# Kernel optimization log

Measured on AMD Instinct MI355X. Metric: run time of the kernel, lower is better.

The kernel has to match this reference:

```python
import jax, jax.numpy as jnp
import numpy as np

IN_CH, EMBED_DIM, N_CODES = 8, 64, 512


def conv1d(x, w, b, stride, pad):
    # x: [B,C,T], w: [O,I,K] (torch Conv1d layout)
    y = jax.lax.conv_general_dilated(x, w, (stride,), [(pad, pad)],
                                     dimension_numbers=('NCH', 'OIH', 'NCH'))
    return y + b[None, :, None]


def conv_transpose1d(x, w, b, stride, pad):
    # w: [I,O,K] (torch ConvTranspose1d layout); equiv to lhs-dilated conv with flipped kernel
    k = w.shape[2]
    wf = jnp.flip(jnp.transpose(w, (1, 0, 2)), axis=2)  # [O,I,K]
    y = jax.lax.conv_general_dilated(x, wf, (1,), [(k - 1 - pad, k - 1 - pad)],
                                     lhs_dilation=(stride,),
                                     dimension_numbers=('NCH', 'OIH', 'NCH'))
    return y + b[None, :, None]


def setup_inputs() -> dict:
    key = jax.random.key(0)
    ks = jax.random.split(key, 16)
    def p(k, shape, fan_in):
        lim = 1.0 / np.sqrt(fan_in)
        return jax.random.uniform(k, shape, jnp.float32, -lim, lim)
    x = jax.random.normal(ks[0], (16, IN_CH, 32768), jnp.float32)
    # encoder convs (torch Conv1d: [out,in,k])
    w1 = p(ks[1], (64, IN_CH, 7), IN_CH * 7);   b1 = p(ks[2], (64,), IN_CH * 7)
    w2 = p(ks[3], (128, 64, 5), 64 * 5);        b2 = p(ks[4], (128,), 64 * 5)
    w3 = p(ks[5], (EMBED_DIM, 128, 3), 128 * 3); b3 = p(ks[6], (EMBED_DIM,), 128 * 3)
    codebook = jax.random.uniform(ks[7], (N_CODES, EMBED_DIM), jnp.float32,
                                  -1.0 / N_CODES, 1.0 / N_CODES)
    # decoder conv-transposes (torch ConvTranspose1d: [in,out,k])
    dw1 = p(ks[8], (EMBED_DIM, 128, 4), EMBED_DIM * 4); db1 = p(ks[9], (128,), EMBED_DIM * 4)
    dw2 = p(ks[10], (128, 64, 4), 128 * 4);             db2 = p(ks[11], (64,), 128 * 4)
    dw3 = p(ks[12], (64, IN_CH, 4), 64 * 4);            db3 = p(ks[13], (IN_CH,), 64 * 4)
    return {'x': x, 'w1': w1, 'b1': b1, 'w2': w2, 'b2': b2, 'w3': w3, 'b3': b3,
            'codebook': codebook, 'dw1': dw1, 'db1': db1, 'dw2': dw2, 'db2': db2,
            'dw3': dw3, 'db3': db3}


def quantize(z_e, codebook):
    # z_e: [B,D,T]
    B, D, T = z_e.shape
    z_flat = jnp.transpose(z_e, (0, 2, 1)).reshape(-1, D)  # [B*T, D]
    # squared euclidean distances [B*T, n_codes]
    d2 = (jnp.sum(z_flat * z_flat, axis=1, keepdims=True)
          - 2.0 * z_flat @ codebook.T
          + jnp.sum(codebook * codebook, axis=1)[None, :])
    indices = jnp.argmin(d2, axis=1)
    z_q = codebook[indices].reshape(B, T, D).transpose(0, 2, 1)  # [B,D,T]
    return z_q, indices.reshape(B, T)


def mse(a, b):
    d = a - b
    return jnp.mean(d * d)


def reference(x, w1, b1, w2, b2, w3, b3, codebook, dw1, db1, dw2, db2, dw3, db3):
    sg = jax.lax.stop_gradient
    z = jax.nn.relu(conv1d(x, w1, b1, 2, 3))
    z = jax.nn.relu(conv1d(z, w2, b2, 2, 2))
    z_e = conv1d(z, w3, b3, 2, 1)  # [B, D, T/8]
    z_q, indices = quantize(z_e, codebook)
    z_q_st = z_e + sg(z_q - z_e)  # straight-through
    r = jax.nn.relu(conv_transpose1d(z_q_st, dw1, db1, 2, 1))
    r = jax.nn.relu(conv_transpose1d(r, dw2, db2, 2, 1))
    x_recon = conv_transpose1d(r, dw3, db3, 2, 1)  # [B, C, T]
    vq_loss = mse(sg(z_q), z_e)
    commitment_loss = mse(sg(z_e), z_q)
    T = min(x.shape[-1], x_recon.shape[-1])
    recon_loss = mse(x_recon[..., :T], x[..., :T])
    conditioning = jnp.mean(z_q_st, axis=-1)  # [B, D]
    return conditioning, vq_loss, commitment_loss, recon_loss
```

## Files before the change

kernel.cpp:

```cpp
#include <hip/hip_runtime.h>
#include <hip/hip_bf16.h>


#define NB 16
#define T0 32768
#define T1 16384
#define T2 8192
#define T3 4096
#define NCODES 512
#define EDIM 64

typedef __attribute__((ext_vector_type(8)))  short short8;
typedef __attribute__((ext_vector_type(16))) float f32x16;
typedef __attribute__((ext_vector_type(16))) unsigned u32x16;
typedef __attribute__((ext_vector_type(4)))  float f32x4;

__device__ __forceinline__ float b2f(short s) {
    unsigned u = ((unsigned)(unsigned short)s) << 16;
    float f; __builtin_memcpy(&f, &u, 4); return f;
}
__device__ __forceinline__ short f2bs(float f) {
    __hip_bfloat16 h = __float2bfloat16(f);
    short s; __builtin_memcpy(&s, &h, 2); return s;
}
__device__ __forceinline__ unsigned f2ord(float s) {
    unsigned u = __float_as_uint(s);
    return u ^ ((unsigned)((int)u >> 31) | 0x80000000u);
}

__device__ __forceinline__ void gload_lds16(const void* g, void* l) {
    __builtin_amdgcn_global_load_lds(
        (const __attribute__((address_space(1))) void*)g,
        (__attribute__((address_space(3))) void*)l, 16, 0, 0);
}

__device__ __forceinline__ float block_sum256(float v) {
    #pragma unroll
    for (int off = 32; off > 0; off >>= 1) v += __shfl_down(v, off, 64);
    __shared__ float red[4];
    int lane = threadIdx.x & 63, wv = threadIdx.x >> 6;
    if (lane == 0) red[wv] = v;
    __syncthreads();
    return red[0] + red[1] + red[2] + red[3];
}

__global__ __launch_bounds__(256, 2)
void conv1_mfma(const float* __restrict__ x, const short* __restrict__ w1b,
                const float* __restrict__ b1, short* __restrict__ y) {
    constexpr int BT = 128, NR = 262;
    __shared__ short lxc[NR * 8];
    __shared__ short lw[64 * 64];
    int tid = threadIdx.x, b = blockIdx.z, t0 = blockIdx.x * BT;
    for (int i = tid; i < 512; i += 256) {
        int oc = i >> 3, c8 = i & 7;
        short8 v = *(const short8*)(w1b + oc * 64 + c8 * 8);
        *(short8*)(lw + oc * 64 + (c8 ^ (oc & 7)) * 8) = v;
    }
    for (int r = tid; r < NR; r += 256) {
        int g = 2 * t0 - 3 + r;
        short8 p;
        bool ok = (unsigned)g < (unsigned)T0;
        #pragma unroll
        for (int ic = 0; ic < 8; ic++) {
            float v = ok ? x[((size_t)b * 8 + ic) * T0 + g] : 0.f;
            p[ic] = f2bs(v);
        }
        *(short8*)(lxc + r * 8) = p;
    }
    __syncthreads();
    int wv = tid >> 6, lane = tid & 63, lm = lane & 31, lk = lane >> 5;
    int ml = wv * 32 + lm;
    f32x16 acc[2];
    #pragma unroll
    for (int oj = 0; oj < 2; oj++)
        #pragma unroll
        for (int r = 0; r < 16; r++) acc[oj][r] = 0.f;
    #pragma unroll
    for (int kc = 0; kc < 4; kc++) {
        int q = kc * 2 + lk;
        short8 a = *(const short8*)(lxc + (2 * ml + q) * 8);
        #pragma unroll
        for (int oj = 0; oj < 2; oj++) {
            int oc = oj * 32 + lm;
            short8 bf = *(const short8*)(lw + oc * 64 + (q ^ (oc & 7)) * 8);
            acc[oj] = __builtin_amdgcn_mfma_f32_32x32x16_bf16(a, bf, acc[oj], 0, 0, 0);
        }
    }
    #pragma unroll
    for (int oj = 0; oj < 2; oj++) {
        int oc = oj * 32 + lm;
        float bs = b1[oc];
        #pragma unroll
        for (int r = 0; r < 16; r++) {
            int t = t0 + wv * 32 + (r & 3) + 8 * (r >> 2) + 4 * lk;
            float v = fmaxf(acc[oj][r] + bs, 0.f);
            y[((size_t)b * T1 + t) * 64 + oc] = f2bs(v);
        }
    }
}

template<int IC, int OC, int OCB, int TAPS, int PAD, int BT, int NW, bool RELU, bool F32OUT>
__global__ __launch_bounds__(NW * 64, 2)
void conv_mfma_fwd(const short* __restrict__ x, const short* __restrict__ wb,
                   const float* __restrict__ bias, void* __restrict__ yout,
                   const short* __restrict__ zb, int Tin, int Tout) {
    constexpr int C8 = IC / 8;
    constexpr int NR = 2 * (BT - 1) + TAPS;
    __shared__ short lw[TAPS * OCB * IC];
    __shared__ short lx[NR * IC];
    const int tid = threadIdx.x;
    const int b   = blockIdx.z;
    const int ocg = blockIdx.y * OCB;
    const int t0  = blockIdx.x * BT;
    const int r0  = 2 * t0 - PAD;
    for (int i = tid; i < TAPS * OCB * C8; i += NW * 64) {
        int tap = i / (OCB * C8), rem = i - tap * OCB * C8;
        int ocl = rem / C8, c8 = rem - ocl * C8;
        short8 v = *(const short8*)(wb + ((size_t)tap * OC + ocg + ocl) * IC + c8 * 8);
        *(short8*)(lw + (tap * OCB + ocl) * IC + (c8 ^ (ocl & (C8 - 1))) * 8) = v;
    }
    const short* xg = x + (size_t)b * Tin * IC;
    for (int idx = tid; idx < NR * C8; idx += NW * 64) {
        int row = idx / C8, c8 = idx - row * C8;
        int gr = r0 + row;
        int sc8 = c8 ^ ((row >> 1) & (C8 - 1));
        const short* src = ((unsigned)gr < (unsigned)Tin)
            ? xg + (size_t)gr * IC + sc8 * 8 : zb;
        gload_lds16(src, lx + idx * 8);
    }
    __syncthreads();

    const int wv = tid >> 6, lane = tid & 63;
    const int tl = wv * 32;
    const int lm = lane & 31, lk = lane >> 5;
    f32x16 acc[OCB / 32];
    #pragma unroll
    for (int oj = 0; oj < OCB / 32; oj++)
        #pragma unroll
        for (int r = 0; r < 16; r++) acc[oj][r] = 0.f;

    #pragma unroll
    for (int tap = 0; tap < TAPS; tap++) {
        #pragma unroll
        for (int kc = 0; kc < IC / 16; kc++) {
            int row = 2 * (tl + lm) + tap;
            int c8  = kc * 2 + lk;
            short8 a = *(const short8*)(lx + row * IC + (c8 ^ ((row >> 1) & (C8 - 1))) * 8);
            #pragma unroll
            for (int oj = 0; oj < OCB / 32; oj++) {
                int ocl = oj * 32 + lm;
                short8 bf = *(const short8*)(lw + (tap * OCB + ocl) * IC +
                                             (c8 ^ (ocl & (C8 - 1))) * 8);
                acc[oj] = __builtin_amdgcn_mfma_f32_32x32x16_bf16(a, bf, acc[oj], 0, 0, 0);
            }
        }
    }
    #pragma unroll
    for (int oj = 0; oj < OCB / 32; oj++) {
        int oc = ocg + oj * 32 + lm;
        float bs = bias[oc];
        #pragma unroll
        for (int r = 0; r < 16; r++) {
            int t = t0 + tl + (r & 3) + 8 * (r >> 2) + 4 * lk;
            float v = acc[oj][r] + bs;
            if (RELU) v = fmaxf(v, 0.f);
            if (F32OUT)
                ((float*)yout)[((size_t)b * Tout + t) * OC + oc] = v;
            else
                ((short*)yout)[((size_t)b * Tout + t) * OC + oc] = f2bs(v);
        }
    }
}

template<int IC, int OC, int OCB, int BT, int NW, bool RELU>
__global__ __launch_bounds__(NW * 64, 2)
void conv_mfma_t(const short* __restrict__ x, const short* __restrict__ wb,
                 const float* __restrict__ bias, short* __restrict__ y,
                 const short* __restrict__ zb, int Tin) {
    constexpr int C8 = IC / 8;
    constexpr int NR = BT + 2;
    __shared__ short lw[4 * OCB * IC];
    __shared__ short lx[NR * IC];
    const int tid = threadIdx.x;
    const int b   = blockIdx.z;
    const int ocg = blockIdx.y * OCB;
    const int m0  = blockIdx.x * BT;
    const int r0  = m0 - 1;
    for (int i = tid; i < 4 * OCB * C8; i += NW * 64) {
        int k = i / (OCB * C8), rem = i - k * OCB * C8;
        int ocl = rem / C8, c8 = rem - ocl * C8;
        short8 v = *(const short8*)(wb + ((size_t)k * OC + ocg + ocl) * IC + c8 * 8);
        *(short8*)(lw + (k * OCB + ocl) * IC + (c8 ^ (ocl & (C8 - 1))) * 8) = v;
    }
    const short* xg = x + (size_t)b * Tin * IC;
    for (int idx = tid; idx < NR * C8; idx += NW * 64) {
        int row = idx / C8, c8 = idx - row * C8;
        int gr = r0 + row;
        int sc8 = c8 ^ ((row >> 1) & (C8 - 1));
        const short* src = ((unsigned)gr < (unsigned)Tin)
            ? xg + (size_t)gr * IC + sc8 * 8 : zb;
        gload_lds16(src, lx + idx * 8);
    }
    __syncthreads();

    const int wv = tid >> 6, lane = tid & 63;
    const int ml = wv * 32;
    const int lm = lane & 31, lk = lane >> 5;
    f32x16 accE[OCB / 32], accO[OCB / 32];
    #pragma unroll
    for (int oj = 0; oj < OCB / 32; oj++)
        #pragma unroll
        for (int r = 0; r < 16; r++) { accE[oj][r] = 0.f; accO[oj][r] = 0.f; }

    #pragma unroll
    for (int kc = 0; kc < IC / 16; kc++) {
        int c8 = kc * 2 + lk;
        int rA = ml + lm;
        short8 a_m1, a_0, a_p1;
        {
            int row = rA;
            a_m1 = *(const short8*)(lx + row * IC + (c8 ^ ((row >> 1) & (C8 - 1))) * 8);
            row = rA + 1;
            a_0  = *(const short8*)(lx + row * IC + (c8 ^ ((row >> 1) & (C8 - 1))) * 8);
            row = rA + 2;
            a_p1 = *(const short8*)(lx + row * IC + (c8 ^ ((row >> 1) & (C8 - 1))) * 8);
        }
        #pragma unroll
        for (int oj = 0; oj < OCB / 32; oj++) {
            int ocl = oj * 32 + lm;
            int sw = (c8 ^ (ocl & (C8 - 1))) * 8;
            short8 w0 = *(const short8*)(lw + ((0 * OCB + ocl) * IC) + sw);
            short8 w1 = *(const short8*)(lw + ((1 * OCB + ocl) * IC) + sw);
            short8 w2 = *(const short8*)(lw + ((2 * OCB + ocl) * IC) + sw);
            short8 w3 = *(const short8*)(lw + ((3 * OCB + ocl) * IC) + sw);
            accE[oj] = __builtin_amdgcn_mfma_f32_32x32x16_bf16(a_0,  w1, accE[oj], 0, 0, 0);
            accE[oj] = __builtin_amdgcn_mfma_f32_32x32x16_bf16(a_m1, w3, accE[oj], 0, 0, 0);
            accO[oj] = __builtin_amdgcn_mfma_f32_32x32x16_bf16(a_p1, w0, accO[oj], 0, 0, 0);
            accO[oj] = __builtin_amdgcn_mfma_f32_32x32x16_bf16(a_0,  w2, accO[oj], 0, 0, 0);
        }
    }
    int Tout = 2 * Tin;
    #pragma unroll
    for (int oj = 0; oj < OCB / 32; oj++) {
        int oc = ocg + oj * 32 + lm;
        float bs = bias[oc];
        #pragma unroll
        for (int r = 0; r < 16; r++) {
            int m = m0 + ml + (r & 3) + 8 * (r >> 2) + 4 * lk;
            float ve = accE[oj][r] + bs;
            float vo = accO[oj][r] + bs;
            if (RELU) { ve = fmaxf(ve, 0.f); vo = fmaxf(vo, 0.f); }
            short* yp = y + ((size_t)b * Tout + 2 * m) * OC + oc;
            yp[0]  = f2bs(ve);
            yp[OC] = f2bs(vo);
        }
    }
}

__global__ __launch_bounds__(256, 2)
void convt3_loss(const short* __restrict__ r2, const short* __restrict__ w3m,
                 const float* __restrict__ db3, const float* __restrict__ x,
                 const short* __restrict__ zb, float* __restrict__ acc) {
    constexpr int BT = 256, NR = 258;
    __shared__ short lr[NR * 64];
    __shared__ short lw[16 * 200];
    __shared__ float lxt[8 * 512];
    int tid = threadIdx.x, b = blockIdx.z, m0 = blockIdx.x * BT;
    for (int i = tid; i < 384; i += 256) {
        int n = i / 24, kc = i - n * 24;
        *(short8*)(lw + n * 200 + kc * 8) = *(const short8*)(w3m + n * 192 + kc * 8);
    }
    const short* rb = r2 + (size_t)b * T1 * 64;
    for (int i = tid; i < NR * 8; i += 256) {
        int r = i >> 3, c8 = i & 7;
        int g = m0 - 1 + r;
        int sc8 = c8 ^ (r & 7);
        const short* src = ((unsigned)g < (unsigned)T1)
            ? rb + (size_t)g * 64 + sc8 * 8 : zb;
        gload_lds16(src, lr + i * 8);
    }
    const float* xb = x + (size_t)b * 8 * T0;
    for (int i = tid; i < 1024; i += 256) {
        int oc = i >> 7, c4 = (i & 127) * 4;
        gload_lds16(xb + (size_t)oc * T0 + 2 * m0 + c4, lxt + i * 4);
    }
    __syncthreads();
    int wv = tid >> 6, lane = tid & 63;
    int row16 = lane & 15, quad = lane >> 4;
    short8 bfr[6];
    #pragma unroll
    for (int kb = 0; kb < 6; kb++)
        bfr[kb] = *(const short8*)(lw + row16 * 200 + kb * 32 + quad * 8);
    f32x4 accv[4];
    #pragma unroll
    for (int rg = 0; rg < 4; rg++) accv[rg] = (f32x4){0.f, 0.f, 0.f, 0.f};
    #pragma unroll
    for (int kb = 0; kb < 6; kb++) {
        int kg = kb * 32 + quad * 8;
        int ro = kg >> 6, c8 = (kg >> 3) & 7;
        #pragma unroll
        for (int rg = 0; rg < 4; rg++) {
            int r = wv * 64 + rg * 16 + row16 + ro;
            short8 a = *(const short8*)(lr + r * 64 + (c8 ^ (r & 7)) * 8);
            accv[rg] = __builtin_amdgcn_mfma_f32_16x16x32_bf16(a, bfr[kb], accv[rg], 0, 0, 0);
        }
    }
    int oc = row16 & 7, par = row16 >> 3;
    float bs = db3[oc];
    float s = 0.f;
    #pragma unroll
    for (int rg = 0; rg < 4; rg++)
        #pragma unroll
        for (int reg = 0; reg < 4; reg++) {
            int ml = wv * 64 + rg * 16 + quad * 4 + reg;
            float v = accv[rg][reg] + bs;
            float d = v - lxt[oc * 512 + 2 * ml + par];
            s += d * d;
        }
    s = block_sum256(s);
    if (tid == 0) atomicAdd(acc + 1, s);
}

__global__ void prep_kernel(const float* __restrict__ cb, const float* __restrict__ w1,
                            const float* __restrict__ w2, const float* __restrict__ w3,
                            const float* __restrict__ dw1, const float* __restrict__ dw2,
                            const float* __restrict__ dw3,
                            float* __restrict__ c2, float* __restrict__ cond,
                            float* __restrict__ acc,
                            short* __restrict__ wb2, short* __restrict__ wb3,
                            short* __restrict__ wT1, short* __restrict__ wT2,
                            short* __restrict__ cbbf, short* __restrict__ w1b,
                            short* __restrict__ w3m, short* __restrict__ zb) {
    int i = blockIdx.x * 256 + threadIdx.x;
    if (i < 8) acc[i] = 0.f;
    if (i < 128) zb[i] = (short)0;
    if (i < 1024) cond[i] = 0.f;
    if (i < NCODES) {
        float s = 0.f;
        #pragma unroll
        for (int d = 0; d < EDIM; d++) { float v = cb[i * EDIM + d]; s += v * v; }
        c2[i] = s;
    }
    if (i < 32768) cbbf[i] = f2bs(cb[i]);
    if (i < 4096) {
        int oc = i >> 6, k = i & 63;
        int ic = k & 7, q = k >> 3;
        w1b[i] = (q < 7) ? f2bs(w1[((size_t)oc * 8 + ic) * 7 + q]) : (short)0;
    }
    if (i < 3072) {
        int n = i / 192, k = i - (i / 192) * 192;
        int oc = n & 7;
        float v = 0.f;
        if (n < 8) {
            if (k < 64)       v = dw3[((size_t)k * 8 + oc) * 4 + 3];
            else if (k < 128) v = dw3[((size_t)(k - 64) * 8 + oc) * 4 + 1];
        } else {
            if (k >= 128)     v = dw3[((size_t)(k - 128) * 8 + oc) * 4 + 0];
            else if (k >= 64) v = dw3[((size_t)(k - 64) * 8 + oc) * 4 + 2];
        }
        w3m[i] = f2bs(v);
    }
    if (i < 40960) {
        int tap = i / 8192, r = i - tap * 8192;
        int oc = r >> 6, ic = r & 63;
        wb2[i] = f2bs(w2[((size_t)oc * 64 + ic) * 5 + tap]);
    }
    if (i < 24576) {
        int tap = i / 8192, r = i - tap * 8192;
        int oc = r >> 7, ic = r & 127;
        wb3[i] = f2bs(w3[((size_t)oc * 128 + ic) * 3 + tap]);
    }
    if (i < 32768) {
        int k = i / 8192, r = i - k * 8192;
        int oc = r >> 6, ic = r & 63;
        wT1[i] = f2bs(dw1[((size_t)ic * 128 + oc) * 4 + k]);
    }
    if (i < 32768) {
        int k = i / 8192, r = i - k * 8192;
        int oc = r >> 7, ic = r & 127;
        wT2[i] = f2bs(dw2[((size_t)ic * 64 + oc) * 4 + k]);
    }
}

__global__ __launch_bounds__(256, 2)
void conv3_quant(const short* __restrict__ a2, const short* __restrict__ wb3,
                 const float* __restrict__ b3, const float* __restrict__ cb,
                 const short* __restrict__ cbbf, const float* __restrict__ c2g,
                 const short* __restrict__ zb, short* __restrict__ zq,
                 float* __restrict__ cond, float* __restrict__ accg) {
    constexpr int IC = 128, C8 = IC / 8;
    constexpr int BT = 128;
    constexpr int NR = 2 * (BT - 1) + 3;
    __shared__ short lx[NR * IC];
    __shared__ float lc2[NCODES];
    __shared__ int   ibuf[BT];
    __shared__ float scr[4 * 64];
    int tid = threadIdx.x, b = blockIdx.z, t0 = blockIdx.x * BT;
    int r0 = 2 * t0 - 1;
    for (int i = tid; i < NCODES; i += 256) lc2[i] = c2g[i];
    const short* xg = a2 + (size_t)b * T2 * IC;
    for (int idx = tid; idx < NR * C8; idx += 256) {
        int row = idx >> 4, c8 = idx & 15;
        int gr = r0 + row;
        int sc8 = c8 ^ ((row >> 1) & 15);
        const short* src = ((unsigned)gr < (unsigned)T2)
            ? xg + (size_t)gr * IC + sc8 * 8 : zb;
        gload_lds16(src, lx + idx * 8);
    }
    __syncthreads();

    int wv = tid >> 6, lane = tid & 63, lm = lane & 31, lk = lane >> 5;
    int tl = wv * 32;
    f32x16 acc[2];
    #pragma unroll
    for (int oj = 0; oj < 2; oj++)
        #pragma unroll
        for (int r = 0; r < 16; r++) acc[oj][r] = 0.f;
    #pragma unroll
    for (int tap = 0; tap < 3; tap++) {
        #pragma unroll
        for (int kc = 0; kc < 8; kc++) {
            int row = 2 * (tl + lm) + tap;
            int c8  = kc * 2 + lk;
            short8 a = *(const short8*)(lx + row * IC + (c8 ^ ((row >> 1) & 15)) * 8);
            #pragma unroll
            for (int oj = 0; oj < 2; oj++) {
                short8 bf = *(const short8*)(wb3 +
                    ((size_t)tap * 64 + oj * 32 + lm) * IC + c8 * 8);
                acc[oj] = __builtin_amdgcn_mfma_f32_32x32x16_bf16(a, bf, acc[oj], 0, 0, 0);
            }
        }
    }
    float bs0 = b3[lm], bs1 = b3[32 + lm];
    #pragma unroll
    for (int r = 0; r < 16; r++) { acc[0][r] += bs0; acc[1][r] += bs1; }
    __syncthreads();

    short* lzq = lx;
    short* lcb = lx + 8192;
    #pragma unroll
    for (int oj = 0; oj < 2; oj++) {
        int oc = oj * 32 + lm;
        #pragma unroll
        for (int r = 0; r < 16; r++) {
            int tloc = tl + (r & 3) + 8 * (r >> 2) + 4 * lk;
            lzq[tloc * 64 + (((oc >> 3) ^ (tloc & 7)) * 8) + (oc & 7)] = f2bs(acc[oj][r]);
        }
    }
    __syncthreads();

    int arow = wv * 32 + lm;
    short8 afr[4];
    #pragma unroll
    for (int kc = 0; kc < 4; kc++) {
        int c8 = kc * 2 + lk;
        afr[kc] = *(const short8*)(lzq + arow * 64 + ((c8 ^ (arow & 7)) * 8));
    }
    u32x16 bestp;
    #pragma unroll
    for (int r = 0; r < 16; r++) bestp[r] = 0xFFFFFFFFu;
    for (int half = 0; half < 2; half++) {
        for (int idx = tid; idx < 2048; idx += 256) {
            int row = idx >> 3, s = idx & 7;
            gload_lds16(cbbf + ((size_t)(half * 256 + row)) * 64 + ((s ^ (row & 7)) * 8),
                        lcb + idx * 8);
        }
        __syncthreads();
        for (int ct8 = 0; ct8 < 8; ct8++) {
            int ct = half * 8 + ct8;
            f32x16 aq;
            #pragma unroll
            for (int r = 0; r < 16; r++) aq[r] = 0.f;
            int row = ct8 * 32 + lm;
            #pragma unroll
            for (int kc = 0; kc < 4; kc++) {
                int s = lk + 2 * kc;
                short8 bf = *(const short8*)(lcb + row * 64 + ((s ^ (row & 7)) * 8));
                aq = __builtin_amdgcn_mfma_f32_32x32x16_bf16(afr[kc], bf, aq, 0, 0, 0);
            }
            unsigned cidx = (unsigned)(ct * 32 + lm);
            float c2v = lc2[cidx];
            #pragma unroll
            for (int r = 0; r < 16; r++) {
                float sd = c2v - 2.f * aq[r];
                unsigned p = (f2ord(sd) & 0xFFFFFE00u) | cidx;
                bestp[r] = (p < bestp[r]) ? p : bestp[r];
            }
        }
        __syncthreads();
    }
    #pragma unroll
    for (int r = 0; r < 16; r++) {
        unsigned p = bestp[r];
        #pragma unroll
        for (int mk = 1; mk < 32; mk <<= 1) {
            unsigned op = (unsigned)__shfl_xor((int)p, mk, 64);
            p = (op < p) ? op : p;
        }
        if (lm == 0) ibuf[wv * 32 + (r & 3) + 8 * (r >> 2) + 4 * lk] = (int)(p & 511u);
    }
    __syncthreads();

    float vql = 0.f, cpart0 = 0.f, cpart1 = 0.f;
    short* zqb = zq + ((size_t)(b * T3 + t0)) * 64;
    #pragma unroll
    for (int r = 0; r < 16; r++) {
        int tloc = tl + (r & 3) + 8 * (r >> 2) + 4 * lk;
        int code = ibuf[tloc];
        const float* cv = cb + (size_t)code * 64;
        float c0 = cv[lm], c1 = cv[32 + lm];
        float d0 = acc[0][r] - c0, d1 = acc[1][r] - c1;
        vql += d0 * d0 + d1 * d1;
        cpart0 += c0; cpart1 += c1;
        zqb[(size_t)tloc * 64 + lm]      = f2bs(c0);
        zqb[(size_t)tloc * 64 + 32 + lm] = f2bs(c1);
    }
    cpart0 += __shfl_down(cpart0, 32, 64);
    cpart1 += __shfl_down(cpart1, 32, 64);
    if (lk == 0) { scr[wv * 64 + lm] = cpart0; scr[wv * 64 + 32 + lm] = cpart1; }
    __syncthreads();
    if (tid < 64) {
        float s = scr[tid] + scr[64 + tid] + scr[128 + tid] + scr[192 + tid];
        atomicAdd(cond + b * 64 + tid, s);
    }
    vql = block_sum256(vql);
    if (tid == 0) atomicAdd(accg, vql);
}

__global__ void fin_kernel(const float* __restrict__ cond,
                           const float* __restrict__ acc, float* __restrict__ out) {
    int i = threadIdx.x;
    out[i] = cond[i] * (1.f / (float)T3);
    if (i == 0) {
        float vq = acc[0] * (1.f / 4194304.f);
        out[1024] = vq;
        out[1025] = vq;
        out[1026] = acc[1] * (1.f / 4194304.f);
    }
}

extern "C" void kernel_launch(void* const* d_in, const int* in_sizes, int n_in,
                              void* d_out, int out_size, void* d_ws, size_t ws_size,
                              hipStream_t stream) {
    const float* x   = (const float*)d_in[0];
    const float* w1  = (const float*)d_in[1];
    const float* b1  = (const float*)d_in[2];
    const float* w2  = (const float*)d_in[3];
    const float* b2  = (const float*)d_in[4];
    const float* w3  = (const float*)d_in[5];
    const float* b3  = (const float*)d_in[6];
    const float* cb  = (const float*)d_in[7];
    const float* dw1 = (const float*)d_in[8];
    const float* db1 = (const float*)d_in[9];
    const float* dw2 = (const float*)d_in[10];
    const float* db2 = (const float*)d_in[11];
    const float* dw3 = (const float*)d_in[12];
    const float* db3 = (const float*)d_in[13];
    float* out = (float*)d_out;

    char* ws = (char*)d_ws;
    short* a1   = (short*)(ws);
    short* a2   = (short*)(ws + 33554432);
    short* zq   = (short*)(ws + 83886080);
    short* wb2  = (short*)(ws + 92274688);
    short* wb3  = (short*)(ws + 92356608);
    short* wT1  = (short*)(ws + 92405760);
    short* wT2  = (short*)(ws + 92471296);
    short* cbbf = (short*)(ws + 92536832);
    short* w1b  = (short*)(ws + 92602368);
    short* w3m  = (short*)(ws + 92610560);
    float* c2   = (float*)(ws + 92616704);
    float* cnd  = (float*)(ws + 92618752);
    float* acc  = (float*)(ws + 92622848);
    short* zb   = (short*)(ws + 92626944);

    prep_kernel<<<160, 256, 0, stream>>>(cb, w1, w2, w3, dw1, dw2, dw3, c2, cnd,
                                         acc, wb2, wb3, wT1, wT2, cbbf, w1b, w3m,
                                         zb);
    conv1_mfma<<<dim3(T1 / 128, 1, NB), 256, 0, stream>>>(x, w1b, b1, a1);
    conv_mfma_fwd<64, 128, 64, 5, 2, 128, 4, true, false>
        <<<dim3(T2 / 128, 2, NB), 256, 0, stream>>>(a1, wb2, b2, a2, zb, T1, T2);
    conv3_quant<<<dim3(T3 / 128, 1, NB), 256, 0, stream>>>(a2, wb3, b3, cb, cbbf,
                                                           c2, zb, zq, cnd, acc);
    conv_mfma_t<64, 128, 64, 128, 4, true>
        <<<dim3(T3 / 128, 2, NB), 256, 0, stream>>>(zq, wT1, db1, a2, zb, T3);
    conv_mfma_t<128, 64, 32, 128, 4, true>
        <<<dim3(T2 / 128, 2, NB), 256, 0, stream>>>(a2, wT2, db2, a1, zb, T2);
    convt3_loss<<<dim3(T1 / 256, 1, NB), 256, 0, stream>>>(a1, w3m, db3, x, zb, acc);
    fin_kernel<<<1, 1024, 0, stream>>>(cnd, acc, out);
}
```

Measured before the change: 221.8 us.

## Loop over output-channel halves in one block to reuse the staged input tile

The conv2 and the two transposed-conv kernels no longer split output channels across blockIdx.y. Each block now stages its input time tile into LDS once and loops over output-channel halves, reloading only the weight slice between halves. Weight staging also switches from register round-trips to direct global-to-LDS async loads. This halves the grid and removes the duplicated input staging, but adds an extra barrier per half, serialises the halves inside each block, and leaves fewer blocks to hide latency.

```diff
diff --git a/kernel.cpp b/kernel.cpp
--- a/kernel.cpp
+++ b/kernel.cpp
@@ -99,26 +99,19 @@
     }
 }
 
-template<int IC, int OC, int OCB, int TAPS, int PAD, int BT, int NW, bool RELU, bool F32OUT>
+template<int IC, int OC, int OCH, int TAPS, int PAD, int BT, int NW, bool RELU, bool F32OUT>
 __global__ __launch_bounds__(NW * 64, 2)
-void conv_mfma_fwd(const short* __restrict__ x, const short* __restrict__ wb,
-                   const float* __restrict__ bias, void* __restrict__ yout,
-                   const short* __restrict__ zb, int Tin, int Tout) {
+void conv_mfma_fwd_full(const short* __restrict__ x, const short* __restrict__ wb,
+                        const float* __restrict__ bias, void* __restrict__ yout,
+                        const short* __restrict__ zb, int Tin, int Tout) {
     constexpr int C8 = IC / 8;
     constexpr int NR = 2 * (BT - 1) + TAPS;
-    __shared__ short lw[TAPS * OCB * IC];
+    __shared__ short lw[TAPS * OCH * IC];
     __shared__ short lx[NR * IC];
     const int tid = threadIdx.x;
     const int b   = blockIdx.z;
-    const int ocg = blockIdx.y * OCB;
     const int t0  = blockIdx.x * BT;
     const int r0  = 2 * t0 - PAD;
-    for (int i = tid; i < TAPS * OCB * C8; i += NW * 64) {
-        int tap = i / (OCB * C8), rem = i - tap * OCB * C8;
-        int ocl = rem / C8, c8 = rem - ocl * C8;
-        short8 v = *(const short8*)(wb + ((size_t)tap * OC + ocg + ocl) * IC + c8 * 8);
-        *(short8*)(lw + (tap * OCB + ocl) * IC + (c8 ^ (ocl & (C8 - 1))) * 8) = v;
-    }
     const short* xg = x + (size_t)b * Tin * IC;
     for (int idx = tid; idx < NR * C8; idx += NW * 64) {
         int row = idx / C8, c8 = idx - row * C8;
@@ -128,70 +121,76 @@
             ? xg + (size_t)gr * IC + sc8 * 8 : zb;
         gload_lds16(src, lx + idx * 8);
     }
-    __syncthreads();
-
     const int wv = tid >> 6, lane = tid & 63;
     const int tl = wv * 32;
     const int lm = lane & 31, lk = lane >> 5;
-    f32x16 acc[OCB / 32];
-    #pragma unroll
-    for (int oj = 0; oj < OCB / 32; oj++)
-        #pragma unroll
-        for (int r = 0; r < 16; r++) acc[oj][r] = 0.f;
-
-    #pragma unroll
-    for (int tap = 0; tap < TAPS; tap++) {
-        #pragma unroll
-        for (int kc = 0; kc < IC / 16; kc++) {
-            int row = 2 * (tl + lm) + tap;
-            int c8  = kc * 2 + lk;
-            short8 a = *(const short8*)(lx + row * IC + (c8 ^ ((row >> 1) & (C8 - 1))) * 8);
-            #pragma unroll
-            for (int oj = 0; oj < OCB / 32; oj++) {
-                int ocl = oj * 32 + lm;
-                short8 bf = *(const short8*)(lw + (tap * OCB + ocl) * IC +
-                                             (c8 ^ (ocl & (C8 - 1))) * 8);
-                acc[oj] = __builtin_amdgcn_mfma_f32_32x32x16_bf16(a, bf, acc[oj], 0, 0, 0);
-            }
-        }
-    }
-    #pragma unroll
-    for (int oj = 0; oj < OCB / 32; oj++) {
-        int oc = ocg + oj * 32 + lm;
-        float bs = bias[oc];
-        #pragma unroll
-        for (int r = 0; r < 16; r++) {
-            int t = t0 + tl + (r & 3) + 8 * (r >> 2) + 4 * lk;
-            float v = acc[oj][r] + bs;
-            if (RELU) v = fmaxf(v, 0.f);
-            if (F32OUT)
-                ((float*)yout)[((size_t)b * Tout + t) * OC + oc] = v;
-            else
-                ((short*)yout)[((size_t)b * Tout + t) * OC + oc] = f2bs(v);
-        }
-    }
-}
-
-template<int IC, int OC, int OCB, int BT, int NW, bool RELU>
+
+    #pragma unroll
+    for (int h = 0; h < OC / OCH; h++) {
+        const int ocg = h * OCH;
+        for (int i = tid; i < TAPS * OCH * C8; i += NW * 64) {
+            int tap = i / (OCH * C8), rem = i - tap * OCH * C8;
+            int ocl = rem / C8, d = rem - ocl * C8;
+            int sc8 = d ^ (ocl & (C8 - 1));
+            gload_lds16(wb + ((size_t)tap * OC + ocg + ocl) * IC + sc8 * 8,
+                        lw + i * 8);
+        }
+        __syncthreads();
+
+        f32x16 acc[OCH / 32];
+        #pragma unroll
+        for (int oj = 0; oj < OCH / 32; oj++)
+            #pragma unroll
+            for (int r = 0; r < 16; r++) acc[oj][r] = 0.f;
+        #pragma unroll
+        for (int tap = 0; tap < TAPS; tap++) {
+            #pragma unroll
+            for (int kc = 0; kc < IC / 16; kc++) {
+                int row = 2 * (tl + lm) + tap;
+                int c8  = kc * 2 + lk;
+                short8 a = *(const short8*)(lx + row * IC +
+                                            (c8 ^ ((row >> 1) & (C8 - 1))) * 8);
+                #pragma unroll
+                for (int oj = 0; oj < OCH / 32; oj++) {
+                    int ocl = oj * 32 + lm;
+                    short8 bf = *(const short8*)(lw + (tap * OCH + ocl) * IC +
+                                                 (c8 ^ (ocl & (C8 - 1))) * 8);
+                    acc[oj] = __builtin_amdgcn_mfma_f32_32x32x16_bf16(a, bf, acc[oj], 0, 0, 0);
+                }
+            }
+        }
+        #pragma unroll
+        for (int oj = 0; oj < OCH / 32; oj++) {
+            int oc = ocg + oj * 32 + lm;
+            float bs = bias[oc];
+            #pragma unroll
+            for (int r = 0; r < 16; r++) {
+                int t = t0 + tl + (r & 3) + 8 * (r >> 2) + 4 * lk;
+                float v = acc[oj][r] + bs;
+                if (RELU) v = fmaxf(v, 0.f);
+                if (F32OUT)
+                    ((float*)yout)[((size_t)b * Tout + t) * OC + oc] = v;
+                else
+                    ((short*)yout)[((size_t)b * Tout + t) * OC + oc] = f2bs(v);
+            }
+        }
+        if (h + 1 < OC / OCH) __syncthreads();
+    }
+}
+
+template<int IC, int OC, int OCH, int BT, int NW, bool RELU>
 __global__ __launch_bounds__(NW * 64, 2)
-void conv_mfma_t(const short* __restrict__ x, const short* __restrict__ wb,
-                 const float* __restrict__ bias, short* __restrict__ y,
-                 const short* __restrict__ zb, int Tin) {
+void conv_mfma_t_full(const short* __restrict__ x, const short* __restrict__ wb,
+                      const float* __restrict__ bias, short* __restrict__ y,
+                      const short* __restrict__ zb, int Tin) {
     constexpr int C8 = IC / 8;
     constexpr int NR = BT + 2;
-    __shared__ short lw[4 * OCB * IC];
+    __shared__ short lw[4 * OCH * IC];
     __shared__ short lx[NR * IC];
     const int tid = threadIdx.x;
     const int b   = blockIdx.z;
-    const int ocg = blockIdx.y * OCB;
     const int m0  = blockIdx.x * BT;
     const int r0  = m0 - 1;
-    for (int i = tid; i < 4 * OCB * C8; i += NW * 64) {
-        int k = i / (OCB * C8), rem = i - k * OCB * C8;
-        int ocl = rem / C8, c8 = rem - ocl * C8;
-        short8 v = *(const short8*)(wb + ((size_t)k * OC + ocg + ocl) * IC + c8 * 8);
-        *(short8*)(lw + (k * OCB + ocl) * IC + (c8 ^ (ocl & (C8 - 1))) * 8) = v;
-    }
     const short* xg = x + (size_t)b * Tin * IC;
     for (int idx = tid; idx < NR * C8; idx += NW * 64) {
         int row = idx / C8, c8 = idx - row * C8;
@@ -201,59 +200,71 @@
             ? xg + (size_t)gr * IC + sc8 * 8 : zb;
         gload_lds16(src, lx + idx * 8);
     }
-    __syncthreads();
-
     const int wv = tid >> 6, lane = tid & 63;
     const int ml = wv * 32;
     const int lm = lane & 31, lk = lane >> 5;
-    f32x16 accE[OCB / 32], accO[OCB / 32];
-    #pragma unroll
-    for (int oj = 0; oj < OCB / 32; oj++)
-        #pragma unroll
-        for (int r = 0; r < 16; r++) { accE[oj][r] = 0.f; accO[oj][r] = 0.f; }
-
-    #pragma unroll
-    for (int kc = 0; kc < IC / 16; kc++) {
-        int c8 = kc * 2 + lk;
-        int rA = ml + lm;
-        short8 a_m1, a_0, a_p1;
-        {
-            int row = rA;
-            a_m1 = *(const short8*)(lx + row * IC + (c8 ^ ((row >> 1) & (C8 - 1))) * 8);
-            row = rA + 1;
-            a_0  = *(const short8*)(lx + row * IC + (c8 ^ ((row >> 1) & (C8 - 1))) * 8);
-            row = rA + 2;
-            a_p1 = *(const short8*)(lx + row * IC + (c8 ^ ((row >> 1) & (C8 - 1))) * 8);
-        }
-        #pragma unroll
-        for (int oj = 0; oj < OCB / 32; oj++) {
-            int ocl = oj * 32 + lm;
-            int sw = (c8 ^ (ocl & (C8 - 1))) * 8;
-            short8 w0 = *(const short8*)(lw + ((0 * OCB + ocl) * IC) + sw);
-            short8 w1 = *(const short8*)(lw + ((1 * OCB + ocl) * IC) + sw);
-            short8 w2 = *(const short8*)(lw + ((2 * OCB + ocl) * IC) + sw);
-            short8 w3 = *(const short8*)(lw + ((3 * OCB + ocl) * IC) + sw);
-            accE[oj] = __builtin_amdgcn_mfma_f32_32x32x16_bf16(a_0,  w1, accE[oj], 0, 0, 0);
-            accE[oj] = __builtin_amdgcn_mfma_f32_32x32x16_bf16(a_m1, w3, accE[oj], 0, 0, 0);
-            accO[oj] = __builtin_amdgcn_mfma_f32_32x32x16_bf16(a_p1, w0, accO[oj], 0, 0, 0);
-            accO[oj] = __builtin_amdgcn_mfma_f32_32x32x16_bf16(a_0,  w2, accO[oj], 0, 0, 0);
-        }
-    }
     int Tout = 2 * Tin;
-    #pragma unroll
-    for (int oj = 0; oj < OCB / 32; oj++) {
-        int oc = ocg + oj * 32 + lm;
-        float bs = bias[oc];
-        #pragma unroll
-        for (int r = 0; r < 16; r++) {
-            int m = m0 + ml + (r & 3) + 8 * (r >> 2) + 4 * lk;
-            float ve = accE[oj][r] + bs;
-            float vo = accO[oj][r] + bs;
-            if (RELU) { ve = fmaxf(ve, 0.f); vo = fmaxf(vo, 0.f); }
-            short* yp = y + ((size_t)b * Tout + 2 * m) * OC + oc;
-            yp[0]  = f2bs(ve);
-            yp[OC] = f2bs(vo);
-        }
+
+    #pragma unroll
+    for (int h = 0; h < OC / OCH; h++) {
+        const int ocg = h * OCH;
+        for (int i = tid; i < 4 * OCH * C8; i += NW * 64) {
+            int k = i / (OCH * C8), rem = i - k * OCH * C8;
+            int ocl = rem / C8, d = rem - ocl * C8;
+            int sc8 = d ^ (ocl & (C8 - 1));
+            gload_lds16(wb + ((size_t)k * OC + ocg + ocl) * IC + sc8 * 8,
+                        lw + i * 8);
+        }
+        __syncthreads();
+
+        f32x16 accE[OCH / 32], accO[OCH / 32];
+        #pragma unroll
+        for (int oj = 0; oj < OCH / 32; oj++)
+            #pragma unroll
+            for (int r = 0; r < 16; r++) { accE[oj][r] = 0.f; accO[oj][r] = 0.f; }
+        #pragma unroll
+        for (int kc = 0; kc < IC / 16; kc++) {
+            int c8 = kc * 2 + lk;
+            int rA = ml + lm;
+            short8 a_m1, a_0, a_p1;
+            {
+                int row = rA;
+                a_m1 = *(const short8*)(lx + row * IC + (c8 ^ ((row >> 1) & (C8 - 1))) * 8);
+                row = rA + 1;
+                a_0  = *(const short8*)(lx + row * IC + (c8 ^ ((row >> 1) & (C8 - 1))) * 8);
+                row = rA + 2;
+                a_p1 = *(const short8*)(lx + row * IC + (c8 ^ ((row >> 1) & (C8 - 1))) * 8);
+            }
+            #pragma unroll
+            for (int oj = 0; oj < OCH / 32; oj++) {
+                int ocl = oj * 32 + lm;
+                int sw = (c8 ^ (ocl & (C8 - 1))) * 8;
+                short8 w0 = *(const short8*)(lw + ((0 * OCH + ocl) * IC) + sw);
+                short8 w1 = *(const short8*)(lw + ((1 * OCH + ocl) * IC) + sw);
+                short8 w2 = *(const short8*)(lw + ((2 * OCH + ocl) * IC) + sw);
+                short8 w3 = *(const short8*)(lw + ((3 * OCH + ocl) * IC) + sw);
+                accE[oj] = __builtin_amdgcn_mfma_f32_32x32x16_bf16(a_0,  w1, accE[oj], 0, 0, 0);
+                accE[oj] = __builtin_amdgcn_mfma_f32_32x32x16_bf16(a_m1, w3, accE[oj], 0, 0, 0);
+                accO[oj] = __builtin_amdgcn_mfma_f32_32x32x16_bf16(a_p1, w0, accO[oj], 0, 0, 0);
+                accO[oj] = __builtin_amdgcn_mfma_f32_32x32x16_bf16(a_0,  w2, accO[oj], 0, 0, 0);
+            }
+        }
+        #pragma unroll
+        for (int oj = 0; oj < OCH / 32; oj++) {
+            int oc = ocg + oj * 32 + lm;
+            float bs = bias[oc];
+            #pragma unroll
+            for (int r = 0; r < 16; r++) {
+                int m = m0 + ml + (r & 3) + 8 * (r >> 2) + 4 * lk;
+                float ve = accE[oj][r] + bs;
+                float vo = accO[oj][r] + bs;
+                if (RELU) { ve = fmaxf(ve, 0.f); vo = fmaxf(vo, 0.f); }
+                short* yp = y + ((size_t)b * Tout + 2 * m) * OC + oc;
+                yp[0]  = f2bs(ve);
+                yp[OC] = f2bs(vo);
+            }
+        }
+        if (h + 1 < OC / OCH) __syncthreads();
     }
 }
 
@@ -578,14 +589,14 @@
                                          acc, wb2, wb3, wT1, wT2, cbbf, w1b, w3m,
                                          zb);
     conv1_mfma<<<dim3(T1 / 128, 1, NB), 256, 0, stream>>>(x, w1b, b1, a1);
-    conv_mfma_fwd<64, 128, 64, 5, 2, 128, 4, true, false>
-        <<<dim3(T2 / 128, 2, NB), 256, 0, stream>>>(a1, wb2, b2, a2, zb, T1, T2);
+    conv_mfma_fwd_full<64, 128, 64, 5, 2, 128, 4, true, false>
+        <<<dim3(T2 / 128, 1, NB), 256, 0, stream>>>(a1, wb2, b2, a2, zb, T1, T2);
     conv3_quant<<<dim3(T3 / 128, 1, NB), 256, 0, stream>>>(a2, wb3, b3, cb, cbbf,
                                                            c2, zb, zq, cnd, acc);
-    conv_mfma_t<64, 128, 64, 128, 4, true>
-        <<<dim3(T3 / 128, 2, NB), 256, 0, stream>>>(zq, wT1, db1, a2, zb, T3);
-    conv_mfma_t<128, 64, 32, 128, 4, true>
-        <<<dim3(T2 / 128, 2, NB), 256, 0, stream>>>(a2, wT2, db2, a1, zb, T2);
+    conv_mfma_t_full<64, 128, 64, 128, 4, true>
+        <<<dim3(T3 / 128, 1, NB), 256, 0, stream>>>(zq, wT1, db1, a2, zb, T3);
+    conv_mfma_t_full<128, 64, 32, 128, 4, true>
+        <<<dim3(T2 / 128, 1, NB), 256, 0, stream>>>(a2, wT2, db2, a1, zb, T2);
     convt3_loss<<<dim3(T1 / 256, 1, NB), 256, 0, stream>>>(a1, w3m, db3, x, zb, acc);
     fin_kernel<<<1, 1024, 0, stream>>>(cnd, acc, out);
 }
```

New measurement: 211.6 us. -4.6%, faster.
